# Performance work log

Measured on AMD Instinct MI355X. Metric: run time of the kernel, lower is better.

## Reference

```python
import jax, jax.numpy as jnp
import numpy as np

BN_EPS = 1e-5


def setup_inputs() -> dict:
    key = jax.random.key(0)
    ks = jax.random.split(key, 3)
    B, S, C, H, W = 4, 8, 64, 96, 96
    P = 6
    DIM = 768
    x = jax.random.normal(ks[0], (B, S, C, H, W), dtype=jnp.float32)
    conv_w = jax.random.normal(ks[1], (C, C, 3, 3), dtype=jnp.float32) * 0.05
    conv_b = jnp.zeros((C,), dtype=jnp.float32)
    bn_gamma = jnp.ones((C,), dtype=jnp.float32)
    bn_beta = jnp.zeros((C,), dtype=jnp.float32)
    bn_mean = jnp.zeros((C,), dtype=jnp.float32)
    bn_var = jnp.ones((C,), dtype=jnp.float32)
    proj_w = jax.random.normal(ks[2], (DIM, P * P * C), dtype=jnp.float32) * 0.02
    proj_b = jnp.zeros((DIM,), dtype=jnp.float32)
    mask = jnp.ones((P, P), dtype=jnp.float32)
    return {"x": x, "conv_w": conv_w, "conv_b": conv_b,
            "bn_gamma": bn_gamma, "bn_beta": bn_beta,
            "bn_mean": bn_mean, "bn_var": bn_var,
            "proj_w": proj_w, "proj_b": proj_b,
            "mask": mask, "patch_size": P}


def reference(x, conv_w, conv_b, bn_gamma, bn_beta, bn_mean, bn_var,
              proj_w, proj_b, mask, patch_size):
    B, S, C, H, W = x.shape
    p = patch_size
    Cout = conv_w.shape[0]
    # Fuse the per-frame loop: run conv over all B*S frames at once.
    xf = x.reshape(B * S, C, H, W)
    y = jax.lax.conv_general_dilated(
        xf, conv_w, window_strides=(1, 1), padding=[(1, 1), (1, 1)],
        dimension_numbers=("NCHW", "OIHW", "NCHW"))
    y = y + conv_b[None, :, None, None]
    # BatchNorm2d (eval-mode running stats); Dropout2d is identity at eval.
    inv = jax.lax.rsqrt(bn_var + BN_EPS)
    y = (y - bn_mean[None, :, None, None]) * (bn_gamma * inv)[None, :, None, None] \
        + bn_beta[None, :, None, None]
    y = jax.nn.gelu(y, approximate=False)  # torch GELU default = exact erf
    y = y.reshape(B, S, Cout, H, W)
    # Patch extraction, row-major over (l_idx, r_idx) exactly as the loop.
    pr = H // p  # patches per row
    patches = y.reshape(B, S, Cout, pr, p, pr, p).transpose(0, 1, 3, 5, 2, 4, 6)
    patches = patches.reshape(B, S, pr * pr, Cout, p, p) * mask  # [B,S,P,C,p,p]
    # Flatten(start_dim=2 on [B,S,C,p,p]) + Linear + GELU, batched over patches.
    flat = patches.reshape(B, S, pr * pr, Cout * p * p)
    tokens = jax.nn.gelu(
        jnp.einsum("bsnf,df->bsnd", flat, proj_w) + proj_b, approximate=False)
    return tokens, patches
```

## Files before the change

### kernel.cpp

```cpp
#include <hip/hip_runtime.h>
#include <hip/hip_bf16.h>
#include <math.h>


typedef unsigned short u16;
typedef __bf16 bf16x8 __attribute__((ext_vector_type(8)));
typedef float f32x4 __attribute__((ext_vector_type(4)));

#define NFRM 32
#define CH 64
#define HW 96
#define HWP 98
#define KP 2304
#define DIMN 768
#define MTOK 8192
#define TOKN (MTOK * DIMN)
#define NPAT (MTOK * KP)
#define XHWC_ELEMS ((size_t)NFRM * HWP * HWP * CH)
#define BP_OFF XHWC_ELEMS
#define PW_OFF (BP_OFF + 36864)
#define ABF_OFF (PW_OFF + 1769472)
#define WS_NEED_FUSED (((size_t)ABF_OFF + (size_t)NPAT) * 2)
#define BSTR 200

static __device__ __forceinline__ u16 f2b(float f) {
  unsigned u = __builtin_bit_cast(unsigned, f);
  u += 0x7fffu + ((u >> 16) & 1u);
  return (u16)(u >> 16);
}
static __device__ __forceinline__ float gelu_f(float x) {
  return 0.5f * x * (1.0f + erff(x * 0.7071067811865476f));
}

typedef __attribute__((address_space(3))) unsigned int lds_uint;
typedef __attribute__((address_space(1))) const unsigned int g_uint;
static __device__ __forceinline__ void gload16(const u16* g, u16* s) {
  __builtin_amdgcn_global_load_lds((g_uint*)g, (lds_uint*)s, 16, 0, 0);
}

__global__ __launch_bounds__(256) void k_halo(u16* __restrict__ xhwc) {
  const int e = blockIdx.x * 256 + threadIdx.x;
  const int g = e & 7;
  const int rest = e >> 3;
  const int p = rest % 388, f = rest / 388;
  int r, c;
  if (p < 98)       { r = 0;       c = p; }
  else if (p < 196) { r = 97;      c = p - 98; }
  else if (p < 292) { r = p - 195; c = 0; }
  else              { r = p - 291; c = 97; }
  *(uint4*)&xhwc[(((size_t)f * HWP + r) * HWP + c) * CH + g * 8] = (uint4){0, 0, 0, 0};
}

__global__ __launch_bounds__(256) void k_transpose(const float* __restrict__ x,
                                                   u16* __restrict__ xhwc) {
  __shared__ u16 tile[96 * 66];
  const int f = blockIdx.x / 96, h = blockIdx.x % 96;
  const int t = threadIdx.x;
  const float* xp = x + (size_t)f * CH * HW * HW + (size_t)h * HW;
#pragma unroll
  for (int k = 0; k < 6; ++k) {
    int e = (k * 256 + t) * 4;
    int ci = e / 96, w = e % 96;
    float4 v = *(const float4*)(xp + (size_t)ci * (HW * HW) + w);
    tile[(w + 0) * 66 + ci] = f2b(v.x);
    tile[(w + 1) * 66 + ci] = f2b(v.y);
    tile[(w + 2) * 66 + ci] = f2b(v.z);
    tile[(w + 3) * 66 + ci] = f2b(v.w);
  }
  __syncthreads();
  u16* op = xhwc + ((size_t)(f * HWP + h + 1) * HWP + 1) * CH;
#pragma unroll
  for (int k = 0; k < 12; ++k) {
    int e2 = (k * 256 + t) * 2;
    int w = e2 >> 6, ci = e2 & 63;
    *(unsigned*)(op + e2) = *(const unsigned*)(&tile[w * 66 + ci]);
  }
}

__global__ __launch_bounds__(256) void k_bpack(const float* __restrict__ w,
                                               u16* __restrict__ bp) {
  int e = blockIdx.x * 256 + threadIdx.x;
  int co = e / 576, r = e - co * 576, tap = r >> 6, ci = r & 63;
  bp[e] = f2b(w[(co * 64 + ci) * 9 + tap]);
}

__global__ __launch_bounds__(256) void k_pw(const float* __restrict__ pw,
                                            u16* __restrict__ dst) {
  int e = (blockIdx.x * 256 + threadIdx.x) * 4;
  float4 v = *(const float4*)(pw + e);
  ushort4 o;
  o.x = f2b(v.x); o.y = f2b(v.y); o.z = f2b(v.z); o.w = f2b(v.w);
  *(ushort4*)(dst + e) = o;
}

__global__ __launch_bounds__(256, 2) void k_conv(
    const u16* __restrict__ xhwc, const u16* __restrict__ bw,
    const float* __restrict__ cb, const float* __restrict__ gma,
    const float* __restrict__ bta, const float* __restrict__ mu,
    const float* __restrict__ var, const float* __restrict__ msk,
    float* __restrict__ pout, u16* __restrict__ abf) {
  __shared__ alignas(16) char SMEM[76800];
  u16* Asm = (u16*)SMEM;
  u16* Bsm = (u16*)(SMEM + 51200);
  float* Fsm = (float*)SMEM;

  const int bx = blockIdx.x;
  const int f = bx >> 5, rem = bx & 31, pr = rem >> 1, half = rem & 1;
  const int t = threadIdx.x, wv = t >> 6, l = t & 63, quad = l >> 4, lm = l & 15;
  const int wm = wv >> 1, wn = wv & 1;

  const u16* sbase = xhwc + (((size_t)f * HWP + pr * 6) * HWP + half * 48) * CH;
  const int pc = l >> 3;
  const int gsw = (l & 7) ^ pc;
  for (int c = wv; c < 50; c += 4) {
    const int p = c * 8 + pc;
    const int row = p / 50, ac = p - row * 50;
    gload16(sbase + ((size_t)row * HWP + ac) * CH + gsw * 8, Asm + c * 512);
  }

  int pb[9];
#pragma unroll
  for (int mf = 0; mf < 9; ++mf) {
    const int i16 = wm * 9 + mf;
    pb[mf] = (i16 / 3) * 50 + (i16 % 3) * 16 + lm;
  }
  f32x4 acc[9][2];
#pragma unroll
  for (int mf = 0; mf < 9; ++mf) {
    acc[mf][0] = (f32x4){0.f, 0.f, 0.f, 0.f};
    acc[mf][1] = (f32x4){0.f, 0.f, 0.f, 0.f};
  }

#pragma unroll
  for (int ph = 0; ph < 3; ++ph) {
    if (ph > 0) __syncthreads();
    for (int e = t; e < 1536; e += 256) {
      const int co = e / 24, kk = e - co * 24;
      *(uint4*)&Bsm[co * BSTR + kk * 8] =
          *(const uint4*)&bw[co * 576 + ph * 192 + kk * 8];
    }
    __syncthreads();
#pragma unroll
    for (int tp = 0; tp < 3; ++tp) {
      const int di = ph, dj = tp;
#pragma unroll
      for (int ks = 0; ks < 2; ++ks) {
        const int kq = ks * 4 + quad;
        const bf16x8 b0 = *(const bf16x8*)&Bsm[(wn * 32 + lm) * BSTR + tp * 64 + ks * 32 + quad * 8];
        const bf16x8 b1 = *(const bf16x8*)&Bsm[(wn * 32 + 16 + lm) * BSTR + tp * 64 + ks * 32 + quad * 8];
#pragma unroll
        for (int mf = 0; mf < 9; ++mf) {
          const int p = pb[mf] + di * 50 + dj;
          const bf16x8 a = *(const bf16x8*)&Asm[p * 64 + ((kq ^ (p & 7)) << 3)];
          acc[mf][0] = __builtin_amdgcn_mfma_f32_16x16x32_bf16(a, b0, acc[mf][0], 0, 0, 0);
          acc[mf][1] = __builtin_amdgcn_mfma_f32_16x16x32_bf16(a, b1, acc[mf][1], 0, 0, 0);
        }
      }
    }
  }

  __syncthreads();
#pragma unroll
  for (int nf = 0; nf < 2; ++nf) {
    const int co = wn * 32 + nf * 16 + lm;
    const float scv = gma[co] * rsqrtf(var[co] + 1e-5f);
    const float b2v = (cb[co] - mu[co]) * scv + bta[co];
#pragma unroll
    for (int mf = 0; mf < 9; ++mf) {
#pragma unroll
      for (int rg = 0; rg < 4; ++rg) {
        const int sp = wm * 144 + mf * 16 + quad * 4 + rg;
        const int orow = sp / 48, oc = sp - orow * 48;
        const int nl = oc / 6, pj = oc - nl * 6;
        const int jj = orow * 6 + pj;
        float v = acc[mf][nf][rg] * scv + b2v;
        v = gelu_f(v) * msk[jj];
        Fsm[nl * 2304 + co * 36 + jj] = v;
      }
    }
  }
  __syncthreads();
  const size_t brow = (size_t)(f * 256 + pr * 16 + half * 8) * KP;
  float* pbase = pout + brow;
#pragma unroll
  for (int k = 0; k < 18; ++k) {
    const int li = t + k * 256;
    *(float4*)&pbase[li * 4] = *(const float4*)&Fsm[li * 4];
  }
  if (abf) {
    u16* adst = abf + brow;
#pragma unroll
    for (int k = 0; k < 18; ++k) {
      const int li = t + k * 256;
      const float4 w = *(const float4*)&Fsm[li * 4];
      ushort4 o;
      o.x = f2b(w.x); o.y = f2b(w.y); o.z = f2b(w.z); o.w = f2b(w.w);
      *(ushort4*)&adst[li * 4] = o;
    }
  }
}

__global__ __launch_bounds__(256) void k_cvt(const float* __restrict__ pat,
                                             u16* __restrict__ abf) {
  int e = (blockIdx.x * 256 + threadIdx.x) * 4;
  float4 v = *(const float4*)(pat + e);
  ushort4 o;
  o.x = f2b(v.x); o.y = f2b(v.y); o.z = f2b(v.z); o.w = f2b(v.w);
  *(ushort4*)(abf + e) = o;
}

__global__ __launch_bounds__(256) void k_gemm(const u16* __restrict__ A,
                                              const u16* __restrict__ Bt,
                                              const float* __restrict__ pb,
                                              float* __restrict__ out) {
  __shared__ u16 As[128 * 40];
  __shared__ u16 Bs[64 * 40];
  const int bn = blockIdx.x % 12, bm = blockIdx.x / 12;
  const int m0 = bm * 128, n0 = bn * 64;
  const int t = threadIdx.x, wv = t >> 6, l = t & 63, quad = l >> 4, lm = l & 15;
  const int ar = t >> 2, ac = (t & 3) * 8;

  f32x4 acc[2][4];
#pragma unroll
  for (int s = 0; s < 2; ++s)
#pragma unroll
    for (int u = 0; u < 4; ++u) acc[s][u] = (f32x4){0.f, 0.f, 0.f, 0.f};

  for (int k0 = 0; k0 < KP; k0 += 32) {
    __syncthreads();
    *(uint4*)&As[ar * 40 + ac] = *(const uint4*)&A[(size_t)(m0 + ar) * KP + k0 + ac];
    *(uint4*)&As[(ar + 64) * 40 + ac] =
        *(const uint4*)&A[(size_t)(m0 + ar + 64) * KP + k0 + ac];
    *(uint4*)&Bs[ar * 40 + ac] = *(const uint4*)&Bt[(size_t)(n0 + ar) * KP + k0 + ac];
    __syncthreads();
    const int ko = quad * 8;
    bf16x8 a0 = *(const bf16x8*)&As[(wv * 32 + lm) * 40 + ko];
    bf16x8 a1 = *(const bf16x8*)&As[(wv * 32 + 16 + lm) * 40 + ko];
#pragma unroll
    for (int u = 0; u < 4; ++u) {
      bf16x8 b = *(const bf16x8*)&Bs[(u * 16 + lm) * 40 + ko];
      acc[0][u] = __builtin_amdgcn_mfma_f32_16x16x32_bf16(a0, b, acc[0][u], 0, 0, 0);
      acc[1][u] = __builtin_amdgcn_mfma_f32_16x16x32_bf16(a1, b, acc[1][u], 0, 0, 0);
    }
  }
#pragma unroll
  for (int u = 0; u < 4; ++u) {
    const int n = n0 + u * 16 + lm;
    const float bias = pb[n];
#pragma unroll
    for (int s = 0; s < 2; ++s) {
#pragma unroll
      for (int rg = 0; rg < 4; ++rg) {
        const int m = m0 + wv * 32 + s * 16 + quad * 4 + rg;
        out[(size_t)m * DIMN + n] = gelu_f(acc[s][u][rg] + bias);
      }
    }
  }
}

extern "C" void kernel_launch(void* const* d_in, const int* in_sizes, int n_in,
                              void* d_out, int out_size, void* d_ws, size_t ws_size,
                              hipStream_t stream) {
  const float* x = (const float*)d_in[0];
  const float* conv_w = (const float*)d_in[1];
  const float* conv_b = (const float*)d_in[2];
  const float* bn_gamma = (const float*)d_in[3];
  const float* bn_beta = (const float*)d_in[4];
  const float* bn_mean = (const float*)d_in[5];
  const float* bn_var = (const float*)d_in[6];
  const float* proj_w = (const float*)d_in[7];
  const float* proj_b = (const float*)d_in[8];
  const float* mask = (const float*)d_in[9];
  float* out = (float*)d_out;
  float* patches = out + TOKN;
  u16* ws = (u16*)d_ws;
  u16* xhwc = ws;
  u16* bp = ws + BP_OFF;
  u16* pw = ws + PW_OFF;

  const bool fused = ws_size >= WS_NEED_FUSED;
  u16* abf = fused ? ws + ABF_OFF : (u16*)nullptr;

  k_halo<<<388, 256, 0, stream>>>(xhwc);
  k_transpose<<<NFRM * HW, 256, 0, stream>>>(x, xhwc);
  k_bpack<<<144, 256, 0, stream>>>(conv_w, bp);
  k_pw<<<1728, 256, 0, stream>>>(proj_w, pw);
  k_conv<<<NFRM * 32, 256, 0, stream>>>(xhwc, bp, conv_b, bn_gamma, bn_beta,
                                        bn_mean, bn_var, mask, patches, abf);
  if (!fused) {
    k_cvt<<<18432, 256, 0, stream>>>(patches, xhwc);
    abf = xhwc;
  }
  k_gemm<<<64 * 12, 256, 0, stream>>>(abf, pw, proj_b, out);
}
```

Measured before the change: 316.7 us.

## Double conv block to 512 threads and stage epilogue output in two passes

The conv kernel now runs 8 waves per block instead of 4. Each wave covers 16 output channels instead of 32, which halves the accumulator registers per thread and doubles the threads per block. The GELU epilogue is applied in registers, and the shared-memory staging of the fp32 patch output is split into two passes of 4 patches each, so the staging fits inside the existing shared buffer, which still holds A/B data. This is meant to raise wave-level parallelism and latency hiding. In exchange it adds an extra barrier pass and duplicates the A-operand LDS reads across more waves.

Measured after the change: 330.2 us. 1.04x slower.

```diff
diff --git a/kernel.cpp b/kernel.cpp
--- a/kernel.cpp
+++ b/kernel.cpp
@@ -93,7 +93,7 @@
   *(ushort4*)(dst + e) = o;
 }
 
-__global__ __launch_bounds__(256, 2) void k_conv(
+__global__ __launch_bounds__(512, 2) void k_conv(
     const u16* __restrict__ xhwc, const u16* __restrict__ bw,
     const float* __restrict__ cb, const float* __restrict__ gma,
     const float* __restrict__ bta, const float* __restrict__ mu,
@@ -107,12 +107,12 @@
   const int bx = blockIdx.x;
   const int f = bx >> 5, rem = bx & 31, pr = rem >> 1, half = rem & 1;
   const int t = threadIdx.x, wv = t >> 6, l = t & 63, quad = l >> 4, lm = l & 15;
-  const int wm = wv >> 1, wn = wv & 1;
+  const int wm = wv >> 2, wn = wv & 3;
 
   const u16* sbase = xhwc + (((size_t)f * HWP + pr * 6) * HWP + half * 48) * CH;
   const int pc = l >> 3;
   const int gsw = (l & 7) ^ pc;
-  for (int c = wv; c < 50; c += 4) {
+  for (int c = wv; c < 50; c += 8) {
     const int p = c * 8 + pc;
     const int row = p / 50, ac = p - row * 50;
     gload16(sbase + ((size_t)row * HWP + ac) * CH + gsw * 8, Asm + c * 512);
@@ -124,17 +124,14 @@
     const int i16 = wm * 9 + mf;
     pb[mf] = (i16 / 3) * 50 + (i16 % 3) * 16 + lm;
   }
-  f32x4 acc[9][2];
-#pragma unroll
-  for (int mf = 0; mf < 9; ++mf) {
-    acc[mf][0] = (f32x4){0.f, 0.f, 0.f, 0.f};
-    acc[mf][1] = (f32x4){0.f, 0.f, 0.f, 0.f};
-  }
+  f32x4 acc[9];
+#pragma unroll
+  for (int mf = 0; mf < 9; ++mf) acc[mf] = (f32x4){0.f, 0.f, 0.f, 0.f};
 
 #pragma unroll
   for (int ph = 0; ph < 3; ++ph) {
     if (ph > 0) __syncthreads();
-    for (int e = t; e < 1536; e += 256) {
+    for (int e = t; e < 1536; e += 512) {
       const int co = e / 24, kk = e - co * 24;
       *(uint4*)&Bsm[co * BSTR + kk * 8] =
           *(const uint4*)&bw[co * 576 + ph * 192 + kk * 8];
@@ -146,23 +143,19 @@
 #pragma unroll
       for (int ks = 0; ks < 2; ++ks) {
         const int kq = ks * 4 + quad;
-        const bf16x8 b0 = *(const bf16x8*)&Bsm[(wn * 32 + lm) * BSTR + tp * 64 + ks * 32 + quad * 8];
-        const bf16x8 b1 = *(const bf16x8*)&Bsm[(wn * 32 + 16 + lm) * BSTR + tp * 64 + ks * 32 + quad * 8];
+        const bf16x8 b = *(const bf16x8*)&Bsm[(wn * 16 + lm) * BSTR + tp * 64 + ks * 32 + quad * 8];
 #pragma unroll
         for (int mf = 0; mf < 9; ++mf) {
           const int p = pb[mf] + di * 50 + dj;
           const bf16x8 a = *(const bf16x8*)&Asm[p * 64 + ((kq ^ (p & 7)) << 3)];
-          acc[mf][0] = __builtin_amdgcn_mfma_f32_16x16x32_bf16(a, b0, acc[mf][0], 0, 0, 0);
-          acc[mf][1] = __builtin_amdgcn_mfma_f32_16x16x32_bf16(a, b1, acc[mf][1], 0, 0, 0);
+          acc[mf] = __builtin_amdgcn_mfma_f32_16x16x32_bf16(a, b, acc[mf], 0, 0, 0);
         }
       }
     }
   }
 
-  __syncthreads();
-#pragma unroll
-  for (int nf = 0; nf < 2; ++nf) {
-    const int co = wn * 32 + nf * 16 + lm;
+  {
+    const int co = wn * 16 + lm;
     const float scv = gma[co] * rsqrtf(var[co] + 1e-5f);
     const float b2v = (cb[co] - mu[co]) * scv + bta[co];
 #pragma unroll
@@ -171,31 +164,52 @@
       for (int rg = 0; rg < 4; ++rg) {
         const int sp = wm * 144 + mf * 16 + quad * 4 + rg;
         const int orow = sp / 48, oc = sp - orow * 48;
-        const int nl = oc / 6, pj = oc - nl * 6;
-        const int jj = orow * 6 + pj;
-        float v = acc[mf][nf][rg] * scv + b2v;
-        v = gelu_f(v) * msk[jj];
-        Fsm[nl * 2304 + co * 36 + jj] = v;
+        const int jj = orow * 6 + (oc - (oc / 6) * 6);
+        float v = acc[mf][rg] * scv + b2v;
+        acc[mf][rg] = gelu_f(v) * msk[jj];
       }
     }
   }
   __syncthreads();
-  const size_t brow = (size_t)(f * 256 + pr * 16 + half * 8) * KP;
-  float* pbase = pout + brow;
-#pragma unroll
-  for (int k = 0; k < 18; ++k) {
-    const int li = t + k * 256;
-    *(float4*)&pbase[li * 4] = *(const float4*)&Fsm[li * 4];
-  }
-  if (abf) {
-    u16* adst = abf + brow;
-#pragma unroll
-    for (int k = 0; k < 18; ++k) {
-      const int li = t + k * 256;
-      const float4 w = *(const float4*)&Fsm[li * 4];
-      ushort4 o;
-      o.x = f2b(w.x); o.y = f2b(w.y); o.z = f2b(w.z); o.w = f2b(w.w);
-      *(ushort4*)&adst[li * 4] = o;
+
+#pragma unroll
+  for (int pass = 0; pass < 2; ++pass) {
+    if (pass) __syncthreads();
+    {
+      const int co = wn * 16 + lm;
+#pragma unroll
+      for (int mf = 0; mf < 9; ++mf) {
+#pragma unroll
+        for (int rg = 0; rg < 4; ++rg) {
+          const int sp = wm * 144 + mf * 16 + quad * 4 + rg;
+          const int orow = sp / 48, oc = sp - orow * 48;
+          const int nl = oc / 6, pj = oc - nl * 6;
+          const int jj = orow * 6 + pj;
+          if ((nl >> 2) == pass)
+            Fsm[(nl & 3) * KP + co * 36 + jj] = acc[mf][rg];
+        }
+      }
+    }
+    __syncthreads();
+    const size_t brow = (size_t)(f * 256 + pr * 16 + half * 8 + pass * 4) * KP;
+    float* pdst = pout + brow;
+#pragma unroll
+    for (int k = 0; k < 5; ++k) {
+      const int li = t + k * 512;
+      if (li < 2304) *(float4*)&pdst[li * 4] = *(const float4*)&Fsm[li * 4];
+    }
+    if (abf) {
+      u16* adst = abf + brow;
+#pragma unroll
+      for (int k = 0; k < 5; ++k) {
+        const int li = t + k * 512;
+        if (li < 2304) {
+          const float4 w = *(const float4*)&Fsm[li * 4];
+          ushort4 o;
+          o.x = f2b(w.x); o.y = f2b(w.y); o.z = f2b(w.z); o.w = f2b(w.w);
+          *(ushort4*)&adst[li * 4] = o;
+        }
+      }
     }
   }
 }
@@ -285,7 +299,7 @@
   k_transpose<<<NFRM * HW, 256, 0, stream>>>(x, xhwc);
   k_bpack<<<144, 256, 0, stream>>>(conv_w, bp);
   k_pw<<<1728, 256, 0, stream>>>(proj_w, pw);
-  k_conv<<<NFRM * 32, 256, 0, stream>>>(xhwc, bp, conv_b, bn_gamma, bn_beta,
+  k_conv<<<NFRM * 32, 512, 0, stream>>>(xhwc, bp, conv_b, bn_gamma, bn_beta,
                                         bn_mean, bn_var, mask, patches, abf);
   if (!fused) {
     k_cvt<<<18432, 256, 0, stream>>>(patches, xhwc);
```

## Deepen GEMM K-tile to 128 with direct-to-LDS loads, XOR swizzle, XCD remap

Applied to the files above, without the earlier changes.

The projection GEMM now stages a 128-wide K slice per iteration instead of 32, which cuts the number of barrier pairs per tile by four. Tiles are filled with a gload16 helper (likely a global-to-LDS direct load) and an XOR-swizzled layout replaces the padded rows to avoid LDS bank conflicts. Block IDs are remapped so that consecutive logical tiles land on the same XCD, improving L2 reuse of A and B. LDS use per block grows substantially, which may lower occupancy, and there is still no double buffering.

Measured after the change: 299.4 us. 1.06x faster.

```diff
diff --git a/kernel.cpp b/kernel.cpp
--- a/kernel.cpp
+++ b/kernel.cpp
@@ -213,12 +213,15 @@
                                               const u16* __restrict__ Bt,
                                               const float* __restrict__ pb,
                                               float* __restrict__ out) {
-  __shared__ u16 As[128 * 40];
-  __shared__ u16 Bs[64 * 40];
-  const int bn = blockIdx.x % 12, bm = blockIdx.x / 12;
+  __shared__ alignas(16) u16 As[128 * 128];
+  __shared__ alignas(16) u16 Bs[64 * 128];
+  const int bid = blockIdx.x;
+  const int logical = (bid & 7) * 96 + (bid >> 3);
+  const int bn = logical % 12, bm = logical / 12;
   const int m0 = bm * 128, n0 = bn * 64;
   const int t = threadIdx.x, wv = t >> 6, l = t & 63, quad = l >> 4, lm = l & 15;
-  const int ar = t >> 2, ac = (t & 3) * 8;
+  const int rl = l >> 4;
+  const int slot = l & 15;
 
   f32x4 acc[2][4];
 #pragma unroll
@@ -226,21 +229,31 @@
 #pragma unroll
     for (int u = 0; u < 4; ++u) acc[s][u] = (f32x4){0.f, 0.f, 0.f, 0.f};
 
-  for (int k0 = 0; k0 < KP; k0 += 32) {
+  for (int k0 = 0; k0 < KP; k0 += 128) {
     __syncthreads();
-    *(uint4*)&As[ar * 40 + ac] = *(const uint4*)&A[(size_t)(m0 + ar) * KP + k0 + ac];
-    *(uint4*)&As[(ar + 64) * 40 + ac] =
-        *(const uint4*)&A[(size_t)(m0 + ar + 64) * KP + k0 + ac];
-    *(uint4*)&Bs[ar * 40 + ac] = *(const uint4*)&Bt[(size_t)(n0 + ar) * KP + k0 + ac];
+    for (int c = wv; c < 48; c += 4) {
+      if (c < 32) {
+        const int row = c * 4 + rl;
+        const int gsw2 = slot ^ (row & 15);
+        gload16(A + (size_t)(m0 + row) * KP + k0 + gsw2 * 8, As + c * 512);
+      } else {
+        const int row = (c - 32) * 4 + rl;
+        const int gsw2 = slot ^ (row & 15);
+        gload16(Bt + (size_t)(n0 + row) * KP + k0 + gsw2 * 8, Bs + (c - 32) * 512);
+      }
+    }
     __syncthreads();
-    const int ko = quad * 8;
-    bf16x8 a0 = *(const bf16x8*)&As[(wv * 32 + lm) * 40 + ko];
-    bf16x8 a1 = *(const bf16x8*)&As[(wv * 32 + 16 + lm) * 40 + ko];
-#pragma unroll
-    for (int u = 0; u < 4; ++u) {
-      bf16x8 b = *(const bf16x8*)&Bs[(u * 16 + lm) * 40 + ko];
-      acc[0][u] = __builtin_amdgcn_mfma_f32_16x16x32_bf16(a0, b, acc[0][u], 0, 0, 0);
-      acc[1][u] = __builtin_amdgcn_mfma_f32_16x16x32_bf16(a1, b, acc[1][u], 0, 0, 0);
+#pragma unroll
+    for (int ks = 0; ks < 4; ++ks) {
+      const int gx = ((ks * 4 + quad) ^ lm) << 3;
+      const bf16x8 a0 = *(const bf16x8*)&As[(wv * 32 + lm) * 128 + gx];
+      const bf16x8 a1 = *(const bf16x8*)&As[(wv * 32 + 16 + lm) * 128 + gx];
+#pragma unroll
+      for (int u = 0; u < 4; ++u) {
+        const bf16x8 b = *(const bf16x8*)&Bs[(u * 16 + lm) * 128 + gx];
+        acc[0][u] = __builtin_amdgcn_mfma_f32_16x16x32_bf16(a0, b, acc[0][u], 0, 0, 0);
+        acc[1][u] = __builtin_amdgcn_mfma_f32_16x16x32_bf16(a1, b, acc[1][u], 0, 0, 0);
+      }
     }
   }
 #pragma unroll
```
